# Kernel tuning notes

Measured on AMD Instinct MI355X. Metric: run time of the kernel, lower is better.

The kernel has to match this reference:

```python
import jax, jax.numpy as jnp
import numpy as np

B, S, D, H = 2, 2048, 1024, 16
DK = D // H


def setup_inputs() -> dict:
    key = jax.random.key(0)
    ks = jax.random.split(key, 11)
    s = 1.0 / np.sqrt(D)
    return {
        "q": jax.random.normal(ks[0], (B, S, D), jnp.float32),
        "k": jax.random.normal(ks[1], (B, S, D), jnp.float32),
        "v": jax.random.normal(ks[2], (B, S, D), jnp.float32),
        "mask": jnp.ones((B, 1, S, S), jnp.int32),
        "Wq": jax.random.normal(ks[3], (D, D), jnp.float32) * s,
        "bq": jnp.zeros((D,), jnp.float32),
        "Wk": jax.random.normal(ks[4], (D, D), jnp.float32) * s,
        "bk": jnp.zeros((D,), jnp.float32),
        "Wv": jax.random.normal(ks[5], (D, D), jnp.float32) * s,
        "bv": jnp.zeros((D,), jnp.float32),
        "Wo": jax.random.normal(ks[6], (D, D), jnp.float32) * s,
        "bo": jnp.zeros((D,), jnp.float32),
    }


def reference(q, k, v, mask, Wq, bq, Wk, bk, Wv, bv, Wo, bo):
    # Note: original torch code calls non-in-place masked_fill and discards the
    # result, so the mask has no mathematical effect; we preserve that.
    qh = (q @ Wq + bq).reshape(B, S, H, DK).transpose(0, 2, 1, 3)  # [B,H,S,DK]
    kh = (k @ Wk + bk).reshape(B, S, H, DK).transpose(0, 2, 1, 3)
    vh = (v @ Wv + bv).reshape(B, S, H, DK).transpose(0, 2, 1, 3)
    scores = jnp.einsum("bhqd,bhkd->bhqk", qh, kh) / jnp.sqrt(jnp.float32(DK))
    attn = jax.nn.softmax(scores, axis=-1)
    out = jnp.einsum("bhqk,bhkd->bhqd", attn, vh)  # [B,H,S,DK]
    out = out.transpose(0, 2, 1, 3).reshape(B, S, D)
    return out @ Wo + bo
```

## Files before the change

### kernel.cpp

```cpp
#include <hip/hip_runtime.h>

#define S_LEN    2048
#define D_MODEL  1024
#define N_HEADS  16
#define HEAD_DIM 64
#define BATCH    2

typedef __bf16 bf16x8 __attribute__((ext_vector_type(8)));
typedef float  floatx4 __attribute__((ext_vector_type(4)));

__device__ __forceinline__ unsigned short f2bf(float f) {
    union { float f; unsigned int u; } v;
    v.f = f;
    unsigned int u = v.u;
    u += 0x7fffu + ((u >> 16) & 1u);
    return (unsigned short)(u >> 16);
}

__device__ __forceinline__ unsigned int pk_rne(float a, float b) {
    union { float f; unsigned int u; } ua, ub;
    ua.f = a; ub.f = b;
    unsigned int x = ua.u + 0x7fffu + ((ua.u >> 16) & 1u);
    unsigned int y = ub.u + 0x7fffu + ((ub.u >> 16) & 1u);
    return __builtin_amdgcn_perm(y, x, 0x07060302);
}

__device__ __forceinline__ void gload_lds16(const unsigned short* g, unsigned short* l) {
    __builtin_amdgcn_global_load_lds(
        (const __attribute__((address_space(1))) void*)(const void*)g,
        (__attribute__((address_space(3))) void*)(void*)l,
        16, 0, 0);
}

struct PrepArgs {
    const float* src[3]; unsigned short* dst[3];
    const float* W[4];   unsigned short* Wt[4];
};

#define CONV_BLOCKS (3 * 4096)

__global__ void prep_kernel(PrepArgs args) {
    const int bid = blockIdx.x;
    if (bid < CONV_BLOCKS) {
        const int t   = bid >> 12;
        const int blk = bid & 4095;
        const int i   = blk * 256 + threadIdx.x;
        float4 f = reinterpret_cast<const float4*>(args.src[t])[i];
        ushort4 o;
        o.x = f2bf(f.x); o.y = f2bf(f.y); o.z = f2bf(f.z); o.w = f2bf(f.w);
        reinterpret_cast<ushort4*>(args.dst[t])[i] = o;
    } else {
        __shared__ unsigned short tile[64][65];
        const int r  = bid - CONV_BLOCKS;
        const int w  = r >> 8;
        const int xy = r & 255;
        const int n0 = (xy & 15) * 64, k0 = (xy >> 4) * 64;
        const float* W = args.W[w];
        unsigned short* Wt = args.Wt[w];
        for (int rep = 0; rep < 16; ++rep) {
            int e = rep * 256 + threadIdx.x;
            int kk = e >> 6, nn = e & 63;
            tile[kk][nn] = f2bf(W[(size_t)(k0 + kk) * D_MODEL + n0 + nn]);
        }
        __syncthreads();
        for (int rep = 0; rep < 16; ++rep) {
            int e = rep * 256 + threadIdx.x;
            int nn = e >> 6, kk = e & 63;
            Wt[(size_t)(n0 + nn) * D_MODEL + k0 + kk] = tile[kk][nn];
        }
    }
}

template <int TM, int TN, int MODE>
__device__ __forceinline__
void gemm_body(const unsigned short* __restrict__ A,
               const unsigned short* __restrict__ Bt,
               const float* __restrict__ bias,
               void* __restrict__ out,
               int m0, int n0, float scale,
               unsigned short* As, unsigned short* Bs) {
    constexpr int MT = TM / 32;
    constexpr int NT = TN / 32;
    const int tid  = threadIdx.x;
    const int wid  = tid >> 6;
    const int lane = tid & 63;

    floatx4 acc[MT][NT];
#pragma unroll
    for (int i = 0; i < MT; ++i)
#pragma unroll
        for (int j = 0; j < NT; ++j) acc[i][j] = (floatx4)0.0f;

    const int srow = lane >> 2;
    const int gch  = (lane & 3) ^ ((srow >> 1) & 3);
    const int wr = (wid >> 1) * (TM / 2);
    const int wc = (wid & 1) * (TN / 2);
    const int fr = lane & 15;
    const int fq = lane >> 4;
    const int swz = (fq ^ ((fr >> 1) & 3)) * 8;

    for (int k0 = 0; k0 < D_MODEL; k0 += 32) {
        if (k0) __syncthreads();
#pragma unroll
        for (int ci = 0; ci < (TM + TN) / 64; ++ci) {
            const int c = wid + ci * 4;
            if (c < TM / 16) {
                const int row = c * 16 + srow;
                gload_lds16(A + (size_t)(m0 + row) * D_MODEL + k0 + gch * 8, As + c * 512);
            } else {
                const int cb = c - TM / 16;
                const int row = cb * 16 + srow;
                gload_lds16(Bt + (size_t)(n0 + row) * D_MODEL + k0 + gch * 8, Bs + cb * 512);
            }
        }
        __syncthreads();

        bf16x8 af[MT], bfv[NT];
#pragma unroll
        for (int t = 0; t < MT; ++t)
            af[t] = *reinterpret_cast<const bf16x8*>(As + (wr + t * 16 + fr) * 32 + swz);
#pragma unroll
        for (int t = 0; t < NT; ++t)
            bfv[t] = *reinterpret_cast<const bf16x8*>(Bs + (wc + t * 16 + fr) * 32 + swz);
#pragma unroll
        for (int mt = 0; mt < MT; ++mt)
#pragma unroll
            for (int nt = 0; nt < NT; ++nt)
                acc[mt][nt] = __builtin_amdgcn_mfma_f32_16x16x32_bf16(af[mt], bfv[nt], acc[mt][nt], 0, 0, 0);
    }

#pragma unroll
    for (int nt = 0; nt < NT; ++nt) {
        const int n = n0 + wc + nt * 16 + fr;
        const float bval = bias[n];
#pragma unroll
        for (int mt = 0; mt < MT; ++mt) {
#pragma unroll
            for (int r = 0; r < 4; ++r) {
                const int m = m0 + wr + mt * 16 + fq * 4 + r;
                const float val = (acc[mt][nt][r] + bval) * scale;
                if (MODE == 2) {
                    reinterpret_cast<float*>(out)[(size_t)m * D_MODEL + n] = val;
                } else {
                    const int b = m >> 11, s = m & (S_LEN - 1);
                    const int h = n >> 6, dk = n & 63;
                    const unsigned short o16 = f2bf(val);
                    if (MODE == 0)
                        reinterpret_cast<unsigned short*>(out)[(((size_t)(b * N_HEADS + h)) * S_LEN + s) * HEAD_DIM + dk] = o16;
                    else
                        reinterpret_cast<unsigned short*>(out)[(((size_t)(b * N_HEADS + h)) * HEAD_DIM + dk) * S_LEN + s] = o16;
                }
            }
        }
    }
}

struct QKVArgs {
    const unsigned short* A[3];
    const unsigned short* Bt[3];
    const float* bias[3];
    unsigned short* out[3];
};

__global__ __launch_bounds__(256)
void qkv_gemm_kernel(QKVArgs args) {
    __shared__ __align__(16) unsigned short As[128 * 32];
    __shared__ __align__(16) unsigned short Bs[128 * 32];
    const int z = blockIdx.z;
    const int m0 = blockIdx.y * 128;
    const int n0 = blockIdx.x * 128;
    if (z == 0)
        gemm_body<128, 128, 0>(args.A[0], args.Bt[0], args.bias[0], args.out[0], m0, n0, 0.18033688011112f, As, Bs);
    else if (z == 1)
        gemm_body<128, 128, 0>(args.A[1], args.Bt[1], args.bias[1], args.out[1], m0, n0, 1.0f, As, Bs);
    else
        gemm_body<128, 128, 1>(args.A[2], args.Bt[2], args.bias[2], args.out[2], m0, n0, 1.0f, As, Bs);
}

__global__ __launch_bounds__(256)
void oproj_gemm_kernel(const unsigned short* __restrict__ A,
                       const unsigned short* __restrict__ Bt,
                       const float* __restrict__ bias,
                       float* __restrict__ out) {
    __shared__ __align__(16) unsigned short As[64 * 32];
    __shared__ __align__(16) unsigned short Bs[128 * 32];
    gemm_body<64, 128, 2>(A, Bt, bias, out, blockIdx.y * 64, blockIdx.x * 128, 1.0f, As, Bs);
}

__global__ __launch_bounds__(256)
void attn_kernel(const unsigned short* __restrict__ qhp,
                 const unsigned short* __restrict__ khp,
                 const unsigned short* __restrict__ vtp,
                 unsigned short* __restrict__ outp) {
    __shared__ __align__(16) unsigned short Ks[2][64 * 64];
    __shared__ __align__(16) unsigned short Vs[2][64 * 64];
    __shared__ __align__(16) unsigned short Ps[4][32 * 72];

    const int tid  = threadIdx.x;
    const int wid  = tid >> 6;
    const int lane = tid & 63;
    const int b = blockIdx.z, h = blockIdx.y;
    const int q0 = blockIdx.x * 128;

    const unsigned short* qbase = qhp + (size_t)(b * N_HEADS + h) * S_LEN * HEAD_DIM;
    const unsigned short* kbase = khp + (size_t)(b * N_HEADS + h) * S_LEN * HEAD_DIM;
    const unsigned short* vbase = vtp + (size_t)(b * N_HEADS + h) * HEAD_DIM * S_LEN;

    const int srow = lane >> 3;
    const int gch  = (lane & 7) ^ srow;
    const int fr = lane & 15;
    const int fq = lane >> 4;
    const int sw7 = fr & 7;

    bf16x8 qf[2][2];
#pragma unroll
    for (int qh2 = 0; qh2 < 2; ++qh2)
#pragma unroll
        for (int kk = 0; kk < 2; ++kk)
            qf[qh2][kk] = *reinterpret_cast<const bf16x8*>(
                qbase + (size_t)(q0 + wid * 32 + qh2 * 16 + fr) * HEAD_DIM + (kk * 4 + fq) * 8);

#pragma unroll
    for (int i = 0; i < 2; ++i) {
        const int c = wid + i * 4;
        const int row = c * 8 + srow;
        gload_lds16(kbase + (size_t)row * HEAD_DIM + gch * 8, Ks[0] + c * 512);
        gload_lds16(vbase + (size_t)row * S_LEN + gch * 8,    Vs[0] + c * 512);
    }

    floatx4 o_acc[2][4];
#pragma unroll
    for (int i = 0; i < 2; ++i)
#pragma unroll
        for (int j = 0; j < 4; ++j) o_acc[i][j] = (floatx4)0.0f;
    float l_sum[2] = {0.0f, 0.0f};

    for (int it = 0; it < S_LEN / 64; ++it) {
        const int p = it & 1;
        __syncthreads();

        if (it + 1 < S_LEN / 64) {
            const int kv1 = (it + 1) * 64;
#pragma unroll
            for (int i = 0; i < 2; ++i) {
                const int c = wid + i * 4;
                const int row = c * 8 + srow;
                gload_lds16(kbase + (size_t)(kv1 + row) * HEAD_DIM + gch * 8, Ks[p ^ 1] + c * 512);
                gload_lds16(vbase + (size_t)row * S_LEN + kv1 + gch * 8,      Vs[p ^ 1] + c * 512);
            }
        }

        floatx4 st[2][4];
#pragma unroll
        for (int i = 0; i < 2; ++i)
#pragma unroll
            for (int j = 0; j < 4; ++j) st[i][j] = (floatx4)0.0f;
#pragma unroll
        for (int nt = 0; nt < 4; ++nt) {
#pragma unroll
            for (int kk = 0; kk < 2; ++kk) {
                bf16x8 kf = *reinterpret_cast<const bf16x8*>(
                    Ks[p] + (nt * 16 + fr) * 64 + (((kk * 4 + fq) ^ sw7) * 8));
                st[0][nt] = __builtin_amdgcn_mfma_f32_16x16x32_bf16(kf, qf[0][kk], st[0][nt], 0, 0, 0);
                st[1][nt] = __builtin_amdgcn_mfma_f32_16x16x32_bf16(kf, qf[1][kk], st[1][nt], 0, 0, 0);
            }
        }

#pragma unroll
        for (int qh2 = 0; qh2 < 2; ++qh2) {
#pragma unroll
            for (int nt = 0; nt < 4; ++nt) {
                float p0 = __builtin_amdgcn_exp2f(st[qh2][nt][0]);
                float p1 = __builtin_amdgcn_exp2f(st[qh2][nt][1]);
                float p2 = __builtin_amdgcn_exp2f(st[qh2][nt][2]);
                float p3 = __builtin_amdgcn_exp2f(st[qh2][nt][3]);
                l_sum[qh2] += (p0 + p1) + (p2 + p3);
                uint2 w;
                w.x = pk_rne(p0, p1);
                w.y = pk_rne(p2, p3);
                *reinterpret_cast<uint2*>(Ps[wid] + (qh2 * 16 + fr) * 72 + nt * 16 + fq * 4) = w;
            }
        }
        __asm__ volatile("s_waitcnt lgkmcnt(0)" ::: "memory");

#pragma unroll
        for (int kk = 0; kk < 2; ++kk) {
            bf16x8 pf0 = *reinterpret_cast<const bf16x8*>(Ps[wid] + (fr)      * 72 + kk * 32 + fq * 8);
            bf16x8 pf1 = *reinterpret_cast<const bf16x8*>(Ps[wid] + (16 + fr) * 72 + kk * 32 + fq * 8);
#pragma unroll
            for (int dt = 0; dt < 4; ++dt) {
                bf16x8 vf = *reinterpret_cast<const bf16x8*>(
                    Vs[p] + (dt * 16 + fr) * 64 + (((kk * 4 + fq) ^ sw7) * 8));
                o_acc[0][dt] = __builtin_amdgcn_mfma_f32_16x16x32_bf16(pf0, vf, o_acc[0][dt], 0, 0, 0);
                o_acc[1][dt] = __builtin_amdgcn_mfma_f32_16x16x32_bf16(pf1, vf, o_acc[1][dt], 0, 0, 0);
            }
        }
    }

#pragma unroll
    for (int qh2 = 0; qh2 < 2; ++qh2) {
        float l = l_sum[qh2];
        l += __shfl_xor(l, 16);
        l += __shfl_xor(l, 32);
        float linv[4];
#pragma unroll
        for (int r = 0; r < 4; ++r)
            linv[r] = __builtin_amdgcn_rcpf(__shfl(l, fq * 4 + r));
#pragma unroll
        for (int dt = 0; dt < 4; ++dt) {
#pragma unroll
            for (int r = 0; r < 4; ++r) {
                const int s  = q0 + wid * 32 + qh2 * 16 + fq * 4 + r;
                const int dk = dt * 16 + fr;
                const float val = o_acc[qh2][dt][r] * linv[r];
                outp[((size_t)(b * S_LEN + s)) * D_MODEL + h * HEAD_DIM + dk] = f2bf(val);
            }
        }
    }
}

extern "C" void kernel_launch(void* const* d_in, const int* in_sizes, int n_in,
                              void* d_out, int out_size, void* d_ws, size_t ws_size,
                              hipStream_t stream) {
    (void)in_sizes; (void)n_in; (void)out_size; (void)ws_size;
    const float* q  = (const float*)d_in[0];
    const float* k  = (const float*)d_in[1];
    const float* v  = (const float*)d_in[2];
    const float* Wq = (const float*)d_in[4];
    const float* bq = (const float*)d_in[5];
    const float* Wk = (const float*)d_in[6];
    const float* bk = (const float*)d_in[7];
    const float* Wv = (const float*)d_in[8];
    const float* bv = (const float*)d_in[9];
    const float* Wo = (const float*)d_in[10];
    const float* bo = (const float*)d_in[11];
    float* out = (float*)d_out;

    char* ws = (char*)d_ws;
    const size_t SZ_ACT = (size_t)BATCH * S_LEN * D_MODEL * 2;
    const size_t SZ_W   = (size_t)D_MODEL * D_MODEL * 2;
    unsigned short* qb   = (unsigned short*)(ws);
    unsigned short* kb   = (unsigned short*)(ws + SZ_ACT);
    unsigned short* vb   = (unsigned short*)(ws + 2 * SZ_ACT);
    unsigned short* Wqt  = (unsigned short*)(ws + 3 * SZ_ACT);
    unsigned short* Wkt  = (unsigned short*)(ws + 3 * SZ_ACT + SZ_W);
    unsigned short* Wvt  = (unsigned short*)(ws + 3 * SZ_ACT + 2 * SZ_W);
    unsigned short* Wot  = (unsigned short*)(ws + 3 * SZ_ACT + 3 * SZ_W);
    unsigned short* qhb  = (unsigned short*)(ws + 3 * SZ_ACT + 4 * SZ_W);
    unsigned short* khb  = (unsigned short*)(ws + 4 * SZ_ACT + 4 * SZ_W);
    unsigned short* vtb  = (unsigned short*)(ws + 5 * SZ_ACT + 4 * SZ_W);
    unsigned short* attn = qb;

    PrepArgs pargs;
    pargs.src[0] = q;  pargs.src[1] = k;  pargs.src[2] = v;
    pargs.dst[0] = qb; pargs.dst[1] = kb; pargs.dst[2] = vb;
    pargs.W[0] = Wq;  pargs.W[1] = Wk;  pargs.W[2] = Wv;  pargs.W[3] = Wo;
    pargs.Wt[0] = Wqt; pargs.Wt[1] = Wkt; pargs.Wt[2] = Wvt; pargs.Wt[3] = Wot;
    prep_kernel<<<dim3(CONV_BLOCKS + 1024), 256, 0, stream>>>(pargs);

    QKVArgs gargs;
    gargs.A[0] = qb;  gargs.A[1] = kb;  gargs.A[2] = vb;
    gargs.Bt[0] = Wqt; gargs.Bt[1] = Wkt; gargs.Bt[2] = Wvt;
    gargs.bias[0] = bq; gargs.bias[1] = bk; gargs.bias[2] = bv;
    gargs.out[0] = qhb; gargs.out[1] = khb; gargs.out[2] = vtb;
    qkv_gemm_kernel<<<dim3(8, 32, 3), 256, 0, stream>>>(gargs);

    attn_kernel<<<dim3(S_LEN / 128, N_HEADS, BATCH), 256, 0, stream>>>(qhb, khb, vtb, attn);

    oproj_gemm_kernel<<<dim3(8, 64), 256, 0, stream>>>(attn, Wot, bo, out);
}
```

Before: 262.3 us.

## Stage GEMM and attention epilogues through LDS and use single-wave attention blocks

GEMM epilogues now write accumulators into shared memory and emit coalesced 16-byte global stores, swapping MFMA operand order so the accumulator layout suits each output layout. The attention kernel becomes one-wave blocks of 32 queries that load K/V fragments straight from global memory instead of a double-buffered LDS pipeline. Row sums are computed with an MFMA against a ones vector rather than shuffles, and the attention output is also staged through LDS for vectorized stores. This targets scattered 2-byte stores and block-level synchronization, but gives up LDS sharing of K/V across waves, so global and L2 traffic for K/V rises.

Result: slower. 317.8 us (+21.2%).

```diff
diff --git a/kernel.cpp b/kernel.cpp
--- a/kernel.cpp
+++ b/kernel.cpp
@@ -31,6 +31,8 @@
         (__attribute__((address_space(3))) void*)(void*)l,
         16, 0, 0);
 }
+
+#define LDS_FENCE() __asm__ volatile("s_waitcnt lgkmcnt(0)" ::: "memory")
 
 struct PrepArgs {
     const float* src[3]; unsigned short* dst[3];
@@ -78,9 +80,11 @@
                const float* __restrict__ bias,
                void* __restrict__ out,
                int m0, int n0, float scale,
-               unsigned short* As, unsigned short* Bs) {
+               unsigned short* smem) {
     constexpr int MT = TM / 32;
     constexpr int NT = TN / 32;
+    unsigned short* As = smem;
+    unsigned short* Bs = smem + TM * 32;
     const int tid  = threadIdx.x;
     const int wid  = tid >> 6;
     const int lane = tid & 63;
@@ -125,32 +129,106 @@
 #pragma unroll
         for (int mt = 0; mt < MT; ++mt)
 #pragma unroll
-            for (int nt = 0; nt < NT; ++nt)
-                acc[mt][nt] = __builtin_amdgcn_mfma_f32_16x16x32_bf16(af[mt], bfv[nt], acc[mt][nt], 0, 0, 0);
-    }
-
-#pragma unroll
-    for (int nt = 0; nt < NT; ++nt) {
-        const int n = n0 + wc + nt * 16 + fr;
-        const float bval = bias[n];
+            for (int nt = 0; nt < NT; ++nt) {
+                if (MODE == 1)
+                    acc[mt][nt] = __builtin_amdgcn_mfma_f32_16x16x32_bf16(af[mt], bfv[nt], acc[mt][nt], 0, 0, 0);
+                else
+                    acc[mt][nt] = __builtin_amdgcn_mfma_f32_16x16x32_bf16(bfv[nt], af[mt], acc[mt][nt], 0, 0, 0);
+            }
+    }
+
+    __syncthreads();
+
+    if (MODE == 0) {
+        unsigned short* rp = smem + wid * 1024;
+        unsigned short* outbf = (unsigned short*)out;
+        float4 b4[NT];
+#pragma unroll
+        for (int nt = 0; nt < NT; ++nt)
+            b4[nt] = *reinterpret_cast<const float4*>(bias + n0 + wc + nt * 16 + fq * 4);
+        const int hh = (n0 + wc) >> 6;
 #pragma unroll
         for (int mt = 0; mt < MT; ++mt) {
 #pragma unroll
-            for (int r = 0; r < 4; ++r) {
-                const int m = m0 + wr + mt * 16 + fq * 4 + r;
-                const float val = (acc[mt][nt][r] + bval) * scale;
-                if (MODE == 2) {
-                    reinterpret_cast<float*>(out)[(size_t)m * D_MODEL + n] = val;
-                } else {
-                    const int b = m >> 11, s = m & (S_LEN - 1);
-                    const int h = n >> 6, dk = n & 63;
-                    const unsigned short o16 = f2bf(val);
-                    if (MODE == 0)
-                        reinterpret_cast<unsigned short*>(out)[(((size_t)(b * N_HEADS + h)) * S_LEN + s) * HEAD_DIM + dk] = o16;
-                    else
-                        reinterpret_cast<unsigned short*>(out)[(((size_t)(b * N_HEADS + h)) * HEAD_DIM + dk) * S_LEN + s] = o16;
+            for (int nt = 0; nt < NT; ++nt) {
+                const float* bb = reinterpret_cast<const float*>(&b4[nt]);
+#pragma unroll
+                for (int p = 0; p < 2; ++p) {
+                    float v0 = (acc[mt][nt][2 * p]     + bb[2 * p])     * scale;
+                    float v1 = (acc[mt][nt][2 * p + 1] + bb[2 * p + 1]) * scale;
+                    *reinterpret_cast<unsigned int*>(rp + fr * 64 + nt * 16 + fq * 4 + 2 * p) = pk_rne(v0, v1);
                 }
             }
+            LDS_FENCE();
+#pragma unroll
+            for (int j = 0; j < 2; ++j) {
+                const int row = (lane >> 3) + j * 8;
+                const int m = m0 + wr + mt * 16 + row;
+                const int b = m >> 11, s = m & (S_LEN - 1);
+                uint4 val = *reinterpret_cast<const uint4*>(rp + row * 64 + (lane & 7) * 8);
+                *reinterpret_cast<uint4*>(outbf + (((size_t)(b * N_HEADS + hh) * S_LEN + s) * HEAD_DIM) + (lane & 7) * 8) = val;
+            }
+            LDS_FENCE();
+        }
+    } else if (MODE == 1) {
+        unsigned short* rp = smem + wid * 1024;
+        unsigned short* outbf = (unsigned short*)out;
+        float bval[NT];
+#pragma unroll
+        for (int nt = 0; nt < NT; ++nt) bval[nt] = bias[n0 + wc + nt * 16 + fr];
+#pragma unroll
+        for (int nt = 0; nt < NT; ++nt) {
+#pragma unroll
+            for (int mt = 0; mt < MT; ++mt) {
+#pragma unroll
+                for (int p = 0; p < 2; ++p) {
+                    float v0 = acc[mt][nt][2 * p]     + bval[nt];
+                    float v1 = acc[mt][nt][2 * p + 1] + bval[nt];
+                    *reinterpret_cast<unsigned int*>(rp + fr * 64 + mt * 16 + fq * 4 + 2 * p) = pk_rne(v0, v1);
+                }
+            }
+            LDS_FENCE();
+#pragma unroll
+            for (int j = 0; j < 2; ++j) {
+                const int row = (lane >> 3) + j * 8;
+                const int n = n0 + wc + nt * 16 + row;
+                const int h = n >> 6, dk = n & 63;
+                const int mch = m0 + wr + (lane & 7) * 8;
+                const int b = mch >> 11, s = mch & (S_LEN - 1);
+                uint4 val = *reinterpret_cast<const uint4*>(rp + row * 64 + (lane & 7) * 8);
+                *reinterpret_cast<uint4*>(outbf + ((size_t)(b * N_HEADS + h) * HEAD_DIM + dk) * S_LEN + s) = val;
+            }
+            LDS_FENCE();
+        }
+    } else {
+        float* rpf = reinterpret_cast<float*>(smem) + wid * 1024;
+        float* outf = (float*)out;
+        float4 b4[NT];
+#pragma unroll
+        for (int nt = 0; nt < NT; ++nt)
+            b4[nt] = *reinterpret_cast<const float4*>(bias + n0 + wc + nt * 16 + fq * 4);
+#pragma unroll
+        for (int mt = 0; mt < MT; ++mt) {
+#pragma unroll
+            for (int nt = 0; nt < NT; ++nt) {
+                const float* bb = reinterpret_cast<const float*>(&b4[nt]);
+#pragma unroll
+                for (int p = 0; p < 2; ++p) {
+                    float2 w;
+                    w.x = acc[mt][nt][2 * p]     + bb[2 * p];
+                    w.y = acc[mt][nt][2 * p + 1] + bb[2 * p + 1];
+                    *reinterpret_cast<float2*>(rpf + fr * 64 + nt * 16 + fq * 4 + 2 * p) = w;
+                }
+            }
+            LDS_FENCE();
+#pragma unroll
+            for (int j = 0; j < 4; ++j) {
+                const int row = (lane >> 4) + j * 4;
+                const int m = m0 + wr + mt * 16 + row;
+                float4 val = *reinterpret_cast<const float4*>(rpf + row * 64 + (lane & 15) * 4);
+                *reinterpret_cast<float4*>(outf + (size_t)m * D_MODEL + n0 + wc + (lane & 15) * 4) = val;
+            }
+            LDS_FENCE();
         }
     }
 }
@@ -164,17 +242,16 @@
 
 __global__ __launch_bounds__(256)
 void qkv_gemm_kernel(QKVArgs args) {
-    __shared__ __align__(16) unsigned short As[128 * 32];
-    __shared__ __align__(16) unsigned short Bs[128 * 32];
+    __shared__ __align__(16) unsigned short smem[8192];
     const int z = blockIdx.z;
     const int m0 = blockIdx.y * 128;
     const int n0 = blockIdx.x * 128;
     if (z == 0)
-        gemm_body<128, 128, 0>(args.A[0], args.Bt[0], args.bias[0], args.out[0], m0, n0, 0.18033688011112f, As, Bs);
+        gemm_body<128, 128, 0>(args.A[0], args.Bt[0], args.bias[0], args.out[0], m0, n0, 0.18033688011112f, smem);
     else if (z == 1)
-        gemm_body<128, 128, 0>(args.A[1], args.Bt[1], args.bias[1], args.out[1], m0, n0, 1.0f, As, Bs);
+        gemm_body<128, 128, 0>(args.A[1], args.Bt[1], args.bias[1], args.out[1], m0, n0, 1.0f, smem);
     else
-        gemm_body<128, 128, 1>(args.A[2], args.Bt[2], args.bias[2], args.out[2], m0, n0, 1.0f, As, Bs);
+        gemm_body<128, 128, 1>(args.A[2], args.Bt[2], args.bias[2], args.out[2], m0, n0, 1.0f, smem);
 }
 
 __global__ __launch_bounds__(256)
@@ -182,35 +259,27 @@
                        const unsigned short* __restrict__ Bt,
                        const float* __restrict__ bias,
                        float* __restrict__ out) {
-    __shared__ __align__(16) unsigned short As[64 * 32];
-    __shared__ __align__(16) unsigned short Bs[128 * 32];
-    gemm_body<64, 128, 2>(A, Bt, bias, out, blockIdx.y * 64, blockIdx.x * 128, 1.0f, As, Bs);
-}
-
-__global__ __launch_bounds__(256)
+    __shared__ __align__(16) unsigned short smem[8192];
+    gemm_body<64, 128, 2>(A, Bt, bias, out, blockIdx.y * 64, blockIdx.x * 128, 1.0f, smem);
+}
+
+__global__ __launch_bounds__(64)
 void attn_kernel(const unsigned short* __restrict__ qhp,
                  const unsigned short* __restrict__ khp,
                  const unsigned short* __restrict__ vtp,
                  unsigned short* __restrict__ outp) {
-    __shared__ __align__(16) unsigned short Ks[2][64 * 64];
-    __shared__ __align__(16) unsigned short Vs[2][64 * 64];
-    __shared__ __align__(16) unsigned short Ps[4][32 * 72];
-
-    const int tid  = threadIdx.x;
-    const int wid  = tid >> 6;
-    const int lane = tid & 63;
+    __shared__ __align__(16) unsigned short Ps[32 * 72];
+
+    const int lane = threadIdx.x;
     const int b = blockIdx.z, h = blockIdx.y;
-    const int q0 = blockIdx.x * 128;
+    const int q0 = blockIdx.x * 32;
 
     const unsigned short* qbase = qhp + (size_t)(b * N_HEADS + h) * S_LEN * HEAD_DIM;
     const unsigned short* kbase = khp + (size_t)(b * N_HEADS + h) * S_LEN * HEAD_DIM;
     const unsigned short* vbase = vtp + (size_t)(b * N_HEADS + h) * HEAD_DIM * S_LEN;
 
-    const int srow = lane >> 3;
-    const int gch  = (lane & 7) ^ srow;
     const int fr = lane & 15;
     const int fq = lane >> 4;
-    const int sw7 = fr & 7;
 
     bf16x8 qf[2][2];
 #pragma unroll
@@ -218,37 +287,36 @@
 #pragma unroll
         for (int kk = 0; kk < 2; ++kk)
             qf[qh2][kk] = *reinterpret_cast<const bf16x8*>(
-                qbase + (size_t)(q0 + wid * 32 + qh2 * 16 + fr) * HEAD_DIM + (kk * 4 + fq) * 8);
-
-#pragma unroll
-    for (int i = 0; i < 2; ++i) {
-        const int c = wid + i * 4;
-        const int row = c * 8 + srow;
-        gload_lds16(kbase + (size_t)row * HEAD_DIM + gch * 8, Ks[0] + c * 512);
-        gload_lds16(vbase + (size_t)row * S_LEN + gch * 8,    Vs[0] + c * 512);
-    }
+                qbase + (size_t)(q0 + qh2 * 16 + fr) * HEAD_DIM + (kk * 4 + fq) * 8);
+
+    bf16x8 ones;
+#pragma unroll
+    for (int i = 0; i < 8; ++i) ones[i] = (__bf16)1.0f;
 
     floatx4 o_acc[2][4];
 #pragma unroll
     for (int i = 0; i < 2; ++i)
 #pragma unroll
         for (int j = 0; j < 4; ++j) o_acc[i][j] = (floatx4)0.0f;
-    float l_sum[2] = {0.0f, 0.0f};
+    floatx4 l_acc[2];
+    l_acc[0] = (floatx4)0.0f; l_acc[1] = (floatx4)0.0f;
 
     for (int it = 0; it < S_LEN / 64; ++it) {
-        const int p = it & 1;
-        __syncthreads();
-
-        if (it + 1 < S_LEN / 64) {
-            const int kv1 = (it + 1) * 64;
-#pragma unroll
-            for (int i = 0; i < 2; ++i) {
-                const int c = wid + i * 4;
-                const int row = c * 8 + srow;
-                gload_lds16(kbase + (size_t)(kv1 + row) * HEAD_DIM + gch * 8, Ks[p ^ 1] + c * 512);
-                gload_lds16(vbase + (size_t)row * S_LEN + kv1 + gch * 8,      Vs[p ^ 1] + c * 512);
-            }
-        }
+        const int kv0 = it * 64;
+
+        bf16x8 kf[4][2], vf[4][2];
+#pragma unroll
+        for (int nt = 0; nt < 4; ++nt)
+#pragma unroll
+            for (int kk = 0; kk < 2; ++kk)
+                kf[nt][kk] = *reinterpret_cast<const bf16x8*>(
+                    kbase + (size_t)(kv0 + nt * 16 + fr) * HEAD_DIM + (kk * 4 + fq) * 8);
+#pragma unroll
+        for (int dt = 0; dt < 4; ++dt)
+#pragma unroll
+            for (int kk = 0; kk < 2; ++kk)
+                vf[dt][kk] = *reinterpret_cast<const bf16x8*>(
+                    vbase + (size_t)(dt * 16 + fr) * S_LEN + kv0 + (kk * 4 + fq) * 8);
 
         floatx4 st[2][4];
 #pragma unroll
@@ -256,66 +324,62 @@
 #pragma unroll
             for (int j = 0; j < 4; ++j) st[i][j] = (floatx4)0.0f;
 #pragma unroll
-        for (int nt = 0; nt < 4; ++nt) {
+        for (int nt = 0; nt < 4; ++nt)
 #pragma unroll
             for (int kk = 0; kk < 2; ++kk) {
-                bf16x8 kf = *reinterpret_cast<const bf16x8*>(
-                    Ks[p] + (nt * 16 + fr) * 64 + (((kk * 4 + fq) ^ sw7) * 8));
-                st[0][nt] = __builtin_amdgcn_mfma_f32_16x16x32_bf16(kf, qf[0][kk], st[0][nt], 0, 0, 0);
-                st[1][nt] = __builtin_amdgcn_mfma_f32_16x16x32_bf16(kf, qf[1][kk], st[1][nt], 0, 0, 0);
-            }
-        }
-
-#pragma unroll
-        for (int qh2 = 0; qh2 < 2; ++qh2) {
+                st[0][nt] = __builtin_amdgcn_mfma_f32_16x16x32_bf16(kf[nt][kk], qf[0][kk], st[0][nt], 0, 0, 0);
+                st[1][nt] = __builtin_amdgcn_mfma_f32_16x16x32_bf16(kf[nt][kk], qf[1][kk], st[1][nt], 0, 0, 0);
+            }
+
+#pragma unroll
+        for (int qh2 = 0; qh2 < 2; ++qh2)
 #pragma unroll
             for (int nt = 0; nt < 4; ++nt) {
                 float p0 = __builtin_amdgcn_exp2f(st[qh2][nt][0]);
                 float p1 = __builtin_amdgcn_exp2f(st[qh2][nt][1]);
                 float p2 = __builtin_amdgcn_exp2f(st[qh2][nt][2]);
                 float p3 = __builtin_amdgcn_exp2f(st[qh2][nt][3]);
-                l_sum[qh2] += (p0 + p1) + (p2 + p3);
                 uint2 w;
                 w.x = pk_rne(p0, p1);
                 w.y = pk_rne(p2, p3);
-                *reinterpret_cast<uint2*>(Ps[wid] + (qh2 * 16 + fr) * 72 + nt * 16 + fq * 4) = w;
-            }
-        }
-        __asm__ volatile("s_waitcnt lgkmcnt(0)" ::: "memory");
+                *reinterpret_cast<uint2*>(Ps + (qh2 * 16 + fr) * 72 + nt * 16 + fq * 4) = w;
+            }
+        LDS_FENCE();
 
 #pragma unroll
         for (int kk = 0; kk < 2; ++kk) {
-            bf16x8 pf0 = *reinterpret_cast<const bf16x8*>(Ps[wid] + (fr)      * 72 + kk * 32 + fq * 8);
-            bf16x8 pf1 = *reinterpret_cast<const bf16x8*>(Ps[wid] + (16 + fr) * 72 + kk * 32 + fq * 8);
+            bf16x8 pf0 = *reinterpret_cast<const bf16x8*>(Ps + (fr)      * 72 + kk * 32 + fq * 8);
+            bf16x8 pf1 = *reinterpret_cast<const bf16x8*>(Ps + (16 + fr) * 72 + kk * 32 + fq * 8);
+            l_acc[0] = __builtin_amdgcn_mfma_f32_16x16x32_bf16(ones, pf0, l_acc[0], 0, 0, 0);
+            l_acc[1] = __builtin_amdgcn_mfma_f32_16x16x32_bf16(ones, pf1, l_acc[1], 0, 0, 0);
 #pragma unroll
             for (int dt = 0; dt < 4; ++dt) {
-                bf16x8 vf = *reinterpret_cast<const bf16x8*>(
-                    Vs[p] + (dt * 16 + fr) * 64 + (((kk * 4 + fq) ^ sw7) * 8));
-                o_acc[0][dt] = __builtin_amdgcn_mfma_f32_16x16x32_bf16(pf0, vf, o_acc[0][dt], 0, 0, 0);
-                o_acc[1][dt] = __builtin_amdgcn_mfma_f32_16x16x32_bf16(pf1, vf, o_acc[1][dt], 0, 0, 0);
+                o_acc[0][dt] = __builtin_amdgcn_mfma_f32_16x16x32_bf16(vf[dt][kk], pf0, o_acc[0][dt], 0, 0, 0);
+                o_acc[1][dt] = __builtin_amdgcn_mfma_f32_16x16x32_bf16(vf[dt][kk], pf1, o_acc[1][dt], 0, 0, 0);
             }
         }
     }
 
 #pragma unroll
     for (int qh2 = 0; qh2 < 2; ++qh2) {
-        float l = l_sum[qh2];
-        l += __shfl_xor(l, 16);
-        l += __shfl_xor(l, 32);
-        float linv[4];
-#pragma unroll
-        for (int r = 0; r < 4; ++r)
-            linv[r] = __builtin_amdgcn_rcpf(__shfl(l, fq * 4 + r));
-#pragma unroll
-        for (int dt = 0; dt < 4; ++dt) {
-#pragma unroll
-            for (int r = 0; r < 4; ++r) {
-                const int s  = q0 + wid * 32 + qh2 * 16 + fq * 4 + r;
-                const int dk = dt * 16 + fr;
-                const float val = o_acc[qh2][dt][r] * linv[r];
-                outp[((size_t)(b * S_LEN + s)) * D_MODEL + h * HEAD_DIM + dk] = f2bf(val);
-            }
-        }
+        const float linv = __builtin_amdgcn_rcpf(l_acc[qh2][0]);
+#pragma unroll
+        for (int dt = 0; dt < 4; ++dt)
+#pragma unroll
+            for (int p = 0; p < 2; ++p) {
+                float v0 = o_acc[qh2][dt][2 * p]     * linv;
+                float v1 = o_acc[qh2][dt][2 * p + 1] * linv;
+                *reinterpret_cast<unsigned int*>(
+                    Ps + (qh2 * 16 + fr) * 72 + dt * 16 + fq * 4 + 2 * p) = pk_rne(v0, v1);
+            }
+    }
+    LDS_FENCE();
+#pragma unroll
+    for (int j = 0; j < 4; ++j) {
+        const int row = (lane >> 3) + j * 8;
+        const int s = q0 + row;
+        uint4 val = *reinterpret_cast<const uint4*>(Ps + row * 72 + (lane & 7) * 8);
+        *reinterpret_cast<uint4*>(outp + ((size_t)(b * S_LEN + s)) * D_MODEL + h * HEAD_DIM + (lane & 7) * 8) = val;
     }
 }
 
@@ -365,7 +429,7 @@
     gargs.out[0] = qhb; gargs.out[1] = khb; gargs.out[2] = vtb;
     qkv_gemm_kernel<<<dim3(8, 32, 3), 256, 0, stream>>>(gargs);
 
-    attn_kernel<<<dim3(S_LEN / 128, N_HEADS, BATCH), 256, 0, stream>>>(qhb, khb, vtb, attn);
+    attn_kernel<<<dim3(S_LEN / 32, N_HEADS, BATCH), 64, 0, stream>>>(qhb, khb, vtb, attn);
 
     oproj_gemm_kernel<<<dim3(8, 64), 256, 0, stream>>>(attn, Wot, bo, out);
 }
```
